# Optimization experiments

Hardware: AMD Instinct MI355X
Metric: run time of the kernel (lower is better)

The kernel has to match this reference:

```python
import jax, jax.numpy as jnp
import numpy as np

N_COARSE = 64  # n_coarse samples per ray
EPS = 1e-8
DELTA_INF = 1e10


def setup_inputs() -> dict:
    key = jax.random.key(0)
    ks = jax.random.split(key, 8)
    B, H = 16384, 256
    near = 2.0 + jax.random.uniform(ks[0], (B, 1), dtype=jnp.float32)
    far = 6.0 + jax.random.uniform(ks[1], (B, 1), dtype=jnp.float32)
    center = jax.random.normal(ks[2], (B, 3), dtype=jnp.float32)
    direction = jax.random.normal(ks[3], (B, 3), dtype=jnp.float32)
    direction = direction / jnp.linalg.norm(direction, axis=-1, keepdims=True)
    # stand-in NeRF field: 3 -> 256 -> 256 -> 4 MLP (rgb + sigma)
    W1 = jax.random.normal(ks[4], (3, H), dtype=jnp.float32) * 0.5
    b1 = jnp.zeros((H,), jnp.float32)
    W2 = jax.random.normal(ks[5], (H, H), dtype=jnp.float32) * (1.0 / np.sqrt(H))
    b2 = jnp.zeros((H,), jnp.float32)
    W3 = jax.random.normal(ks[6], (H, 4), dtype=jnp.float32) * (1.0 / np.sqrt(H))
    b3 = jnp.zeros((4,), jnp.float32)
    return {"near": near, "far": far, "center": center, "direction": direction,
            "W1": W1, "b1": b1, "W2": W2, "b2": b2, "W3": W3, "b3": b3}


def reference(near, far, center, direction, W1, b1, W2, b2, W3, b3):
    B = near.shape[0]
    K = N_COARSE
    # sample_coarse: stratified z values, lindisp=False, perturb=0
    z_steps = jnp.linspace(0.0, 1.0, K, dtype=near.dtype)[None, :]          # (1, K)
    z_vals = near * (1.0 - z_steps) + far * z_steps                          # (B, K)
    # composite(): deltas with infinite last interval
    deltas = jnp.concatenate(
        [z_vals[:, 1:] - z_vals[:, :-1],
         jnp.full((B, 1), DELTA_INF, dtype=z_vals.dtype)], axis=-1)          # (B, K)
    # world-space sample points along each ray
    points = center[:, None, :] + z_vals[:, :, None] * direction[:, None, :]  # (B, K, 3)
    # model(points) -> (B, K, 4): rgb + sigma
    h = jax.nn.relu(points @ W1 + b1)
    h = jax.nn.relu(h @ W2 + b2)
    out = h @ W3 + b3
    rgbs = out[..., :3]                                                      # (B, K, 3)
    sigmas = out[..., 3]                                                     # (B, K)
    sigmas_last = sigmas[:, -1]
    # alpha compositing (noise_std=0, training=False -> no noise)
    alphas = 1.0 - jnp.exp(-deltas * jax.nn.relu(sigmas))                    # (B, K)
    alphas_shifted = jnp.concatenate(
        [jnp.ones((B, 1), alphas.dtype), 1.0 - alphas + EPS], axis=-1)       # (B, K+1)
    T = jnp.cumprod(alphas_shifted, axis=-1)                                 # transmittance
    weights = alphas * T[:, :-1]                                             # (B, K)
    rgb_final = jnp.sum(weights[..., None] * rgbs, axis=-2)                  # (B, 3)
    depth_final = jnp.sum(weights * z_vals, axis=-1)                         # (B,)
    # white background: rgb += 1 - accumulated alpha
    pix_alpha = jnp.sum(weights, axis=1)
    rgb_final = rgb_final + 1.0 - pix_alpha[:, None]
    return rgb_final, depth_final, weights, sigmas_last
```

## Files before the change

### kernel.cpp

```cpp
#include <hip/hip_runtime.h>
#include <hip/hip_bf16.h>


constexpr int H  = 256;
constexpr int KS = 64;

typedef __attribute__((ext_vector_type(8))) short short8;
typedef __attribute__((ext_vector_type(4))) float f32x4;

__device__ __forceinline__ f32x4 mfma16(short8 a, short8 b, f32x4 c) {
    return __builtin_amdgcn_mfma_f32_16x16x32_bf16(a, b, c, 0, 0, 0);
}
__device__ __forceinline__ void split_bf16(float x, short& hi, short& lo) {
    __hip_bfloat16 h = __float2bfloat16(x);
    float hf = __bfloat162float(h);
    __hip_bfloat16 l = __float2bfloat16(x - hf);
    union { __hip_bfloat16 b; short s; } c1, c2;
    c1.b = h; c2.b = l;
    hi = c1.s; lo = c2.s;
}
__device__ __forceinline__ unsigned short f2bf(float x) {
    union { __hip_bfloat16 b; unsigned short s; } c;
    c.b = __float2bfloat16(x);
    return c.s;
}
__device__ __forceinline__ float bf2f(unsigned short s) {
    union { unsigned int u; float f; } c;
    c.u = ((unsigned int)s) << 16;
    return c.f;
}

__global__ void pack_w2_kernel(const float* __restrict__ W2,
                               unsigned short* __restrict__ hi,
                               unsigned short* __restrict__ lo)
{
    const int i  = blockIdx.x * 256 + threadIdx.x;
    const int e  = i & 7;
    const int l  = (i >> 3) & 63;
    const int nt = (i >> 9) & 15;
    const int ks = i >> 13;
    const int k  = ks * 32 + (l >> 4) * 8 + e;
    const int n  = nt * 16 + (l & 15);
    short h, lw;
    split_bf16(W2[k * H + n], h, lw);
    hi[i] = (unsigned short)h;
    lo[i] = (unsigned short)lw;
}

struct ABfrags {
    unsigned short ah[8 * 4 * 64 * 8];
    unsigned short al3[8 * 64 * 8];
};
union StageU { ABfrags ab; unsigned short h2f[8 * 4 * 64 * 8]; };

__launch_bounds__(512, 6)
__global__ void nerf_mfma_kernel(
    const float* __restrict__ g_near, const float* __restrict__ g_far,
    const float* __restrict__ g_center, const float* __restrict__ g_dir,
    const float* __restrict__ W1, const float* __restrict__ b1,
    const float* __restrict__ b2,
    const float* __restrict__ W3, const float* __restrict__ b3,
    const unsigned short* __restrict__ w2h, const unsigned short* __restrict__ w2l,
    float* __restrict__ out, int B)
{
    __shared__ __align__(16) StageU u;
    __shared__ __align__(16) float pts[KS][4];
    __shared__ __align__(16) float comb[8][KS][4];
    __shared__ __align__(16) float row63[H];

    const int t    = threadIdx.x;
    const int lane = t & 63;
    const int wv   = __builtin_amdgcn_readfirstlane(t >> 6);
    const int r    = blockIdx.x;

    if (t < KS) {
        const float nr = g_near[r], fa = g_far[r];
        const float uu = (float)t * (1.0f / 63.0f);
        const float z  = nr * (1.0f - uu) + fa * uu;
        pts[t][0] = g_center[r*3+0] + z * g_dir[r*3+0];
        pts[t][1] = g_center[r*3+1] + z * g_dir[r*3+1];
        pts[t][2] = g_center[r*3+2] + z * g_dir[r*3+2];
        pts[t][3] = z;
    }
    __syncthreads();

    {
        const int kbase = wv * 32 + (lane >> 4) * 8;
        float w1r[3][8], b1r[8];
        #pragma unroll
        for (int c = 0; c < 3; ++c) {
            const f32x4 a = *(const f32x4*)&W1[c * H + kbase];
            const f32x4 b = *(const f32x4*)&W1[c * H + kbase + 4];
            #pragma unroll
            for (int e = 0; e < 4; ++e) { w1r[c][e] = a[e]; w1r[c][e+4] = b[e]; }
        }
        {
            const f32x4 a = *(const f32x4*)&b1[kbase];
            const f32x4 b = *(const f32x4*)&b1[kbase + 4];
            #pragma unroll
            for (int e = 0; e < 4; ++e) { b1r[e] = a[e]; b1r[e+4] = b[e]; }
        }
        const int prow = lane & 15;
        #pragma unroll
        for (int mt = 0; mt < 4; ++mt) {
            const f32x4 pt = *(const f32x4*)&pts[mt * 16 + prow][0];
            short8 hv, lv;
            #pragma unroll
            for (int e = 0; e < 8; ++e) {
                float x = fmaf(pt[0], w1r[0][e],
                          fmaf(pt[1], w1r[1][e],
                          fmaf(pt[2], w1r[2][e], b1r[e])));
                x = fmaxf(x, 0.0f);
                const unsigned short hb = f2bf(x);
                hv[e] = (short)hb;
                if (mt == 3) lv[e] = (short)f2bf(x - bf2f(hb));
            }
            *(short8*)&u.ab.ah[((wv * 4 + mt) * 64 + lane) * 8] = hv;
            if (mt == 3) *(short8*)&u.ab.al3[(wv * 64 + lane) * 8] = lv;
        }
    }
    __syncthreads();

    f32x4 acc[4][2];
    #pragma unroll
    for (int mt = 0; mt < 4; ++mt) {
        acc[mt][0] = (f32x4){0.f,0.f,0.f,0.f};
        acc[mt][1] = (f32x4){0.f,0.f,0.f,0.f};
    }
    {
        const int ntg0 = wv * 2, ntg1 = ntg0 + 1;
        const short8* Bh = (const short8*)w2h;
        const short8* Bl = (const short8*)w2l;
        const short8* Ah = (const short8*)u.ab.ah;
        const short8* Al = (const short8*)u.ab.al3;
        __builtin_amdgcn_s_setprio(1);
        #pragma unroll 2
        for (int ks = 0; ks < 8; ++ks) {
            const short8 b0h  = Bh[(ks * 16 + ntg0) * 64 + lane];
            const short8 b0l  = Bl[(ks * 16 + ntg0) * 64 + lane];
            const short8 b1h_ = Bh[(ks * 16 + ntg1) * 64 + lane];
            const short8 b1l_ = Bl[(ks * 16 + ntg1) * 64 + lane];
            #pragma unroll
            for (int mt = 0; mt < 4; ++mt) {
                const short8 ah = Ah[(ks * 4 + mt) * 64 + lane];
                f32x4 c0 = acc[mt][0], c1 = acc[mt][1];
                c0 = mfma16(ah, b0h, c0);
                c0 = mfma16(ah, b0l, c0);
                c1 = mfma16(ah, b1h_, c1);
                c1 = mfma16(ah, b1l_, c1);
                if (mt == 3) {
                    const short8 al = Al[ks * 64 + lane];
                    c0 = mfma16(al, b0h, c0);
                    c1 = mfma16(al, b1h_, c1);
                }
                acc[mt][0] = c0; acc[mt][1] = c1;
            }
        }
        __builtin_amdgcn_s_setprio(0);
    }
    __syncthreads();

    {
        const int c0 = wv * 32 + (lane & 15);
        const int c1 = c0 + 16;
        const float b2c0 = b2[c0], b2c1 = b2[c1];
        const int rlow = (lane >> 4) * 4;
        const int jj0 = lane & 15, jj1 = jj0 + 16;
        const bool lastGrp = ((lane >> 4) == 3);
        #pragma unroll
        for (int mt = 0; mt < 4; ++mt) {
            const f32x4 v0 = acc[mt][0], v1 = acc[mt][1];
            #pragma unroll
            for (int q = 0; q < 4; ++q) {
                const float a0 = fmaxf(v0[q] + b2c0, 0.0f);
                const float a1 = fmaxf(v1[q] + b2c1, 0.0f);
                const int l20 = ((jj0 >> 3) << 4) | (rlow + q);
                const int l21 = ((jj1 >> 3) << 4) | (rlow + q);
                u.h2f[((wv * 4 + mt) * 64 + l20) * 8 + (jj0 & 7)] = f2bf(a0);
                u.h2f[((wv * 4 + mt) * 64 + l21) * 8 + (jj1 & 7)] = f2bf(a1);
                if (mt == 3 && lastGrp && q == 3) { row63[c0] = a0; row63[c1] = a1; }
            }
        }
    }
    __syncthreads();

    {
        const int n = lane & 15;
        short8 bw3;
        #pragma unroll
        for (int e = 0; e < 8; ++e) {
            const int k = wv * 32 + (lane >> 4) * 8 + e;
            const float v = (n < 4) ? W3[k * 4 + n] : 0.0f;
            bw3[e] = (short)f2bf(v);
        }
        const short8* Ah2 = (const short8*)u.h2f;
        #pragma unroll
        for (int mt = 0; mt < 4; ++mt) {
            const short8 a = Ah2[(wv * 4 + mt) * 64 + lane];
            f32x4 d = (f32x4){0.f,0.f,0.f,0.f};
            d = mfma16(a, bw3, d);
            if (n < 4) {
                #pragma unroll
                for (int q = 0; q < 4; ++q)
                    comb[wv][mt * 16 + (lane >> 4) * 4 + q][n] = d[q];
            }
        }
    }
    __syncthreads();

    if (t < KS) {
        const int s = t;

        float sp = 0.f;
        #pragma unroll
        for (int q = 0; q < 4; ++q) {
            const int j = s * 4 + q;
            sp = fmaf(row63[j], W3[j * 4 + 3], sp);
        }
        #pragma unroll
        for (int off = 32; off > 0; off >>= 1) sp += __shfl_xor(sp, off, 64);
        const float sig63 = sp + b3[3];

        f32x4 oo = (f32x4){0.f,0.f,0.f,0.f};
        #pragma unroll
        for (int q = 0; q < 8; ++q) {
            const f32x4 c = *(const f32x4*)&comb[q][s][0];
            oo[0] += c[0]; oo[1] += c[1]; oo[2] += c[2]; oo[3] += c[3];
        }
        const float o0 = oo[0] + b3[0];
        const float o1 = oo[1] + b3[1];
        const float o2 = oo[2] + b3[2];
        const float sigma = (s == 63) ? sig63 : (oo[3] + b3[3]);

        const float z  = pts[s][3];
        const float zn = __shfl_down(z, 1, 64);
        const float delta = (s == 63) ? 1e10f : (zn - z);
        const float alpha = 1.0f - __expf(-delta * fmaxf(sigma, 0.0f));

        float P = 1.0f - alpha + 1e-8f;
        #pragma unroll
        for (int off = 1; off < 64; off <<= 1) {
            const float v = __shfl_up(P, off, 64);
            if (s >= off) P *= v;
        }
        float T = __shfl_up(P, 1, 64);
        if (s == 0) T = 1.0f;
        const float w = alpha * T;

        out[(size_t)B * 4 + (size_t)r * 64 + s] = w;

        float ws = w, dep = w * z, q0 = w * o0, q1 = w * o1, q2 = w * o2;
        #pragma unroll
        for (int off = 32; off > 0; off >>= 1) {
            ws  += __shfl_xor(ws,  off, 64);
            dep += __shfl_xor(dep, off, 64);
            q0  += __shfl_xor(q0,  off, 64);
            q1  += __shfl_xor(q1,  off, 64);
            q2  += __shfl_xor(q2,  off, 64);
        }
        if (s == 0) {
            out[(size_t)r * 3 + 0] = q0 + 1.0f - ws;
            out[(size_t)r * 3 + 1] = q1 + 1.0f - ws;
            out[(size_t)r * 3 + 2] = q2 + 1.0f - ws;
            out[(size_t)B * 3 + r] = dep;
            out[(size_t)B * 68 + r] = sig63;
        }
    }
}

extern "C" void kernel_launch(void* const* d_in, const int* in_sizes, int n_in,
                              void* d_out, int out_size, void* d_ws, size_t ws_size,
                              hipStream_t stream)
{
    const int B = in_sizes[0];
    if (ws_size < (size_t)(2 * 65536 * sizeof(unsigned short))) return;

    unsigned short* w2h = (unsigned short*)d_ws;
    unsigned short* w2l = w2h + 65536;

    pack_w2_kernel<<<256, 256, 0, stream>>>((const float*)d_in[6], w2h, w2l);

    nerf_mfma_kernel<<<B, 512, 0, stream>>>(
        (const float*)d_in[0], (const float*)d_in[1],
        (const float*)d_in[2], (const float*)d_in[3],
        (const float*)d_in[4], (const float*)d_in[5],
        (const float*)d_in[7],
        (const float*)d_in[8], (const float*)d_in[9],
        w2h, w2l,
        (float*)d_out, B);
}
```

Before: 280.1 us.

## Shrink LDS footprint via unions and shared atomics to raise occupancy

Result: slower. 344.7 us (+23.1%).

```diff
diff --git a/kernel.cpp b/kernel.cpp
--- a/kernel.cpp
+++ b/kernel.cpp
@@ -47,13 +47,16 @@
     lo[i] = (unsigned short)lw;
 }
 
-struct ABfrags {
-    unsigned short ah[8 * 4 * 64 * 8];
-    unsigned short al3[8 * 64 * 8];
+struct R2a { unsigned short al3[8 * 64 * 8]; };
+struct R2b { float comb[KS][4]; float row63[H]; };
+union  R2  { R2a a; R2b b; };
+struct SM {
+    union { unsigned short ah[8 * 4 * 64 * 8];
+            unsigned short h2f[8 * 4 * 64 * 8]; } big;
+    R2 r2;
 };
-union StageU { ABfrags ab; unsigned short h2f[8 * 4 * 64 * 8]; };
-
-__launch_bounds__(512, 6)
+
+__launch_bounds__(512, 8)
 __global__ void nerf_mfma_kernel(
     const float* __restrict__ g_near, const float* __restrict__ g_far,
     const float* __restrict__ g_center, const float* __restrict__ g_dir,
@@ -63,26 +66,16 @@
     const unsigned short* __restrict__ w2h, const unsigned short* __restrict__ w2l,
     float* __restrict__ out, int B)
 {
-    __shared__ __align__(16) StageU u;
-    __shared__ __align__(16) float pts[KS][4];
-    __shared__ __align__(16) float comb[8][KS][4];
-    __shared__ __align__(16) float row63[H];
+    __shared__ __align__(16) SM sm;
 
     const int t    = threadIdx.x;
     const int lane = t & 63;
     const int wv   = __builtin_amdgcn_readfirstlane(t >> 6);
     const int r    = blockIdx.x;
 
-    if (t < KS) {
-        const float nr = g_near[r], fa = g_far[r];
-        const float uu = (float)t * (1.0f / 63.0f);
-        const float z  = nr * (1.0f - uu) + fa * uu;
-        pts[t][0] = g_center[r*3+0] + z * g_dir[r*3+0];
-        pts[t][1] = g_center[r*3+1] + z * g_dir[r*3+1];
-        pts[t][2] = g_center[r*3+2] + z * g_dir[r*3+2];
-        pts[t][3] = z;
-    }
-    __syncthreads();
+    const float nr = g_near[r], fa = g_far[r];
+    const float cx = g_center[r*3+0], cy = g_center[r*3+1], cz = g_center[r*3+2];
+    const float dx = g_dir[r*3+0],    dy = g_dir[r*3+1],    dz = g_dir[r*3+2];
 
     {
         const int kbase = wv * 32 + (lane >> 4) * 8;
@@ -103,20 +96,23 @@
         const int prow = lane & 15;
         #pragma unroll
         for (int mt = 0; mt < 4; ++mt) {
-            const f32x4 pt = *(const f32x4*)&pts[mt * 16 + prow][0];
+            const int srow = mt * 16 + prow;
+            const float uu = (float)srow * (1.0f / 63.0f);
+            const float z  = nr * (1.0f - uu) + fa * uu;
+            const float px = cx + z * dx, py = cy + z * dy, pz = cz + z * dz;
             short8 hv, lv;
             #pragma unroll
             for (int e = 0; e < 8; ++e) {
-                float x = fmaf(pt[0], w1r[0][e],
-                          fmaf(pt[1], w1r[1][e],
-                          fmaf(pt[2], w1r[2][e], b1r[e])));
+                float x = fmaf(px, w1r[0][e],
+                          fmaf(py, w1r[1][e],
+                          fmaf(pz, w1r[2][e], b1r[e])));
                 x = fmaxf(x, 0.0f);
                 const unsigned short hb = f2bf(x);
                 hv[e] = (short)hb;
                 if (mt == 3) lv[e] = (short)f2bf(x - bf2f(hb));
             }
-            *(short8*)&u.ab.ah[((wv * 4 + mt) * 64 + lane) * 8] = hv;
-            if (mt == 3) *(short8*)&u.ab.al3[(wv * 64 + lane) * 8] = lv;
+            *(short8*)&sm.big.ah[((wv * 4 + mt) * 64 + lane) * 8] = hv;
+            if (mt == 3) *(short8*)&sm.r2.a.al3[(wv * 64 + lane) * 8] = lv;
         }
     }
     __syncthreads();
@@ -131,26 +127,26 @@
         const int ntg0 = wv * 2, ntg1 = ntg0 + 1;
         const short8* Bh = (const short8*)w2h;
         const short8* Bl = (const short8*)w2l;
-        const short8* Ah = (const short8*)u.ab.ah;
-        const short8* Al = (const short8*)u.ab.al3;
+        const short8* Ah = (const short8*)sm.big.ah;
+        const short8* Al = (const short8*)sm.r2.a.al3;
         __builtin_amdgcn_s_setprio(1);
         #pragma unroll 2
         for (int ks = 0; ks < 8; ++ks) {
             const short8 b0h  = Bh[(ks * 16 + ntg0) * 64 + lane];
-            const short8 b0l  = Bl[(ks * 16 + ntg0) * 64 + lane];
             const short8 b1h_ = Bh[(ks * 16 + ntg1) * 64 + lane];
-            const short8 b1l_ = Bl[(ks * 16 + ntg1) * 64 + lane];
             #pragma unroll
             for (int mt = 0; mt < 4; ++mt) {
                 const short8 ah = Ah[(ks * 4 + mt) * 64 + lane];
                 f32x4 c0 = acc[mt][0], c1 = acc[mt][1];
                 c0 = mfma16(ah, b0h, c0);
-                c0 = mfma16(ah, b0l, c0);
                 c1 = mfma16(ah, b1h_, c1);
-                c1 = mfma16(ah, b1l_, c1);
                 if (mt == 3) {
-                    const short8 al = Al[ks * 64 + lane];
+                    const short8 b0l = Bl[(ks * 16 + ntg0) * 64 + lane];
+                    const short8 b1l = Bl[(ks * 16 + ntg1) * 64 + lane];
+                    const short8 al  = Al[ks * 64 + lane];
+                    c0 = mfma16(ah, b0l, c0);
                     c0 = mfma16(al, b0h, c0);
+                    c1 = mfma16(ah, b1l, c1);
                     c1 = mfma16(al, b1h_, c1);
                 }
                 acc[mt][0] = c0; acc[mt][1] = c1;
@@ -160,6 +156,7 @@
     }
     __syncthreads();
 
+    if (t < 256) ((float*)sm.r2.b.comb)[t] = 0.0f;
     {
         const int c0 = wv * 32 + (lane & 15);
         const int c1 = c0 + 16;
@@ -176,9 +173,11 @@
                 const float a1 = fmaxf(v1[q] + b2c1, 0.0f);
                 const int l20 = ((jj0 >> 3) << 4) | (rlow + q);
                 const int l21 = ((jj1 >> 3) << 4) | (rlow + q);
-                u.h2f[((wv * 4 + mt) * 64 + l20) * 8 + (jj0 & 7)] = f2bf(a0);
-                u.h2f[((wv * 4 + mt) * 64 + l21) * 8 + (jj1 & 7)] = f2bf(a1);
-                if (mt == 3 && lastGrp && q == 3) { row63[c0] = a0; row63[c1] = a1; }
+                sm.big.h2f[((wv * 4 + mt) * 64 + l20) * 8 + (jj0 & 7)] = f2bf(a0);
+                sm.big.h2f[((wv * 4 + mt) * 64 + l21) * 8 + (jj1 & 7)] = f2bf(a1);
+                if (mt == 3 && lastGrp && q == 3) {
+                    sm.r2.b.row63[c0] = a0; sm.r2.b.row63[c1] = a1;
+                }
             }
         }
     }
@@ -193,7 +192,7 @@
             const float v = (n < 4) ? W3[k * 4 + n] : 0.0f;
             bw3[e] = (short)f2bf(v);
         }
-        const short8* Ah2 = (const short8*)u.h2f;
+        const short8* Ah2 = (const short8*)sm.big.h2f;
         #pragma unroll
         for (int mt = 0; mt < 4; ++mt) {
             const short8 a = Ah2[(wv * 4 + mt) * 64 + lane];
@@ -202,7 +201,7 @@
             if (n < 4) {
                 #pragma unroll
                 for (int q = 0; q < 4; ++q)
-                    comb[wv][mt * 16 + (lane >> 4) * 4 + q][n] = d[q];
+                    atomicAdd(&sm.r2.b.comb[mt * 16 + (lane >> 4) * 4 + q][n], d[q]);
             }
         }
     }
@@ -215,26 +214,23 @@
         #pragma unroll
         for (int q = 0; q < 4; ++q) {
             const int j = s * 4 + q;
-            sp = fmaf(row63[j], W3[j * 4 + 3], sp);
+            sp = fmaf(sm.r2.b.row63[j], W3[j * 4 + 3], sp);
         }
         #pragma unroll
         for (int off = 32; off > 0; off >>= 1) sp += __shfl_xor(sp, off, 64);
         const float sig63 = sp + b3[3];
 
-        f32x4 oo = (f32x4){0.f,0.f,0.f,0.f};
-        #pragma unroll
-        for (int q = 0; q < 8; ++q) {
-            const f32x4 c = *(const f32x4*)&comb[q][s][0];
-            oo[0] += c[0]; oo[1] += c[1]; oo[2] += c[2]; oo[3] += c[3];
-        }
-        const float o0 = oo[0] + b3[0];
-        const float o1 = oo[1] + b3[1];
-        const float o2 = oo[2] + b3[2];
-        const float sigma = (s == 63) ? sig63 : (oo[3] + b3[3]);
-
-        const float z  = pts[s][3];
-        const float zn = __shfl_down(z, 1, 64);
-        const float delta = (s == 63) ? 1e10f : (zn - z);
+        const f32x4 cc = *(const f32x4*)&sm.r2.b.comb[s][0];
+        const float o0 = cc[0] + b3[0];
+        const float o1 = cc[1] + b3[1];
+        const float o2 = cc[2] + b3[2];
+        const float sigma = (s == 63) ? sig63 : (cc[3] + b3[3]);
+
+        const float uu = (float)s * (1.0f / 63.0f);
+        const float z  = nr * (1.0f - uu) + fa * uu;
+        const float u2 = (float)(s + 1) * (1.0f / 63.0f);
+        const float z2 = nr * (1.0f - u2) + fa * u2;
+        const float delta = (s == 63) ? 1e10f : (z2 - z);
         const float alpha = 1.0f - __expf(-delta * fmaxf(sigma, 0.0f));
 
         float P = 1.0f - alpha + 1e-8f;
```
